# Kernel optimization log

Hardware: AMD Instinct MI355X
Metric: run time of the kernel (lower is better)

## Reference

```python
import jax, jax.numpy as jnp
import numpy as np

B, N, D = 2, 2048, 1024
H, DH = 16, 64
EPS = 1e-5


def _layernorm(t, g, b):
    m = jnp.mean(t, axis=-1, keepdims=True)
    v = jnp.mean(jnp.square(t - m), axis=-1, keepdims=True)
    return (t - m) * jax.lax.rsqrt(v + EPS) * g + b


def setup_inputs() -> dict:
    key = jax.random.key(0)
    ks = jax.random.split(key, 4)
    return {
        "x": jax.random.normal(ks[0], (B, N, D), dtype=jnp.float32),
        "ln_g": jnp.ones((D,), jnp.float32),
        "ln_b": jnp.zeros((D,), jnp.float32),
        "lnc_g": jnp.ones((D,), jnp.float32),
        "lnc_b": jnp.zeros((D,), jnp.float32),
        "Wq": jax.random.normal(ks[1], (D, H * DH), jnp.float32) * 0.02,
        "Wkv": jax.random.normal(ks[2], (D, 2 * H * DH), jnp.float32) * 0.02,
        "Wo": jax.random.normal(ks[3], (H * DH, D), jnp.float32) * 0.02,
    }


def reference(x, ln_g, ln_b, lnc_g, lnc_b, Wq, Wkv, Wo):
    scale = DH ** (-0.5)
    xn = _layernorm(x, ln_g, ln_b)          # self-attn: context = x
    cn = _layernorm(x, lnc_g, lnc_b)
    q = xn @ Wq                              # [b, n, h*d]
    kv = cn @ Wkv
    k, v = jnp.split(kv, 2, axis=-1)
    # b n (h d) -> b h n d
    q = q.reshape(B, N, H, DH).transpose(0, 2, 1, 3)
    k = k.reshape(B, N, H, DH).transpose(0, 2, 1, 3)
    v = v.reshape(B, N, H, DH).transpose(0, 2, 1, 3)
    sim = jnp.einsum("bhnd,bhmd->bhnm", q, k) * scale
    neg = -jnp.finfo(sim.dtype).max
    causal = jnp.tril(jnp.ones((N, N), dtype=bool))  # allow j <= i
    sim = jnp.where(causal[None, None], sim, neg)
    attn = jax.nn.softmax(sim.astype(jnp.float32), axis=-1)
    out = jnp.einsum("bhnm,bhmd->bhnd", attn, v)
    out = out.transpose(0, 2, 1, 3).reshape(B, N, H * DH)
    return out @ Wo
```

## Files before the change

### kernel.cpp

```cpp
#include <hip/hip_runtime.h>

#define B_  2
#define N_  2048
#define D_  1024
#define H_  16
#define DH_ 64
#define BN_ROWS (B_ * N_)
#define EPS_ 1e-5f
#define QKV_N 3072

typedef __attribute__((ext_vector_type(8))) short bf16x8_t;
typedef __attribute__((ext_vector_type(4))) float f32x4_t;

typedef const unsigned int __attribute__((address_space(1)))* gas_ptr;
typedef unsigned int __attribute__((address_space(3)))* las_ptr;

__device__ __forceinline__ void async16(const unsigned short* g, unsigned short* l) {
    __builtin_amdgcn_global_load_lds((gas_ptr)g, (las_ptr)l, 16, 0, 0);
}

__device__ __forceinline__ unsigned short f2bf(float f) {
    unsigned int u = __float_as_uint(f);
    unsigned int r = u + 0x7FFFu + ((u >> 16) & 1u);
    return (unsigned short)(r >> 16);
}

__global__ __launch_bounds__(256) void ln_dual_kernel(
    const float* __restrict__ x,
    const float* __restrict__ g1, const float* __restrict__ b1,
    const float* __restrict__ g2, const float* __restrict__ b2,
    unsigned short* __restrict__ xn, unsigned short* __restrict__ cn) {
    const int row = blockIdx.x;
    const int tid = threadIdx.x;
    const float4 v = ((const float4*)(x + (size_t)row * D_))[tid];

    float s  = v.x + v.y + v.z + v.w;
    float s2 = v.x * v.x + v.y * v.y + v.z * v.z + v.w * v.w;
    #pragma unroll
    for (int off = 32; off > 0; off >>= 1) {
        s  += __shfl_down(s,  off);
        s2 += __shfl_down(s2, off);
    }
    __shared__ float red[8];
    if ((tid & 63) == 0) { red[tid >> 6] = s; red[4 + (tid >> 6)] = s2; }
    __syncthreads();
    const float S  = red[0] + red[1] + red[2] + red[3];
    const float S2 = red[4] + red[5] + red[6] + red[7];
    const float mean = S * (1.0f / D_);
    const float var  = S2 * (1.0f / D_) - mean * mean;
    const float rstd = rsqrtf(var + EPS_);

    const float4 G1 = ((const float4*)g1)[tid];
    const float4 B1 = ((const float4*)b1)[tid];
    const float4 G2 = ((const float4*)g2)[tid];
    const float4 B2 = ((const float4*)b2)[tid];

    float nx[4] = { (v.x - mean) * rstd, (v.y - mean) * rstd,
                    (v.z - mean) * rstd, (v.w - mean) * rstd };
    ushort4 o1, o2;
    o1.x = f2bf(nx[0] * G1.x + B1.x); o1.y = f2bf(nx[1] * G1.y + B1.y);
    o1.z = f2bf(nx[2] * G1.z + B1.z); o1.w = f2bf(nx[3] * G1.w + B1.w);
    o2.x = f2bf(nx[0] * G2.x + B2.x); o2.y = f2bf(nx[1] * G2.y + B2.y);
    o2.z = f2bf(nx[2] * G2.z + B2.z); o2.w = f2bf(nx[3] * G2.w + B2.w);
    ((ushort4*)(xn + (size_t)row * D_))[tid] = o1;
    ((ushort4*)(cn + (size_t)row * D_))[tid] = o2;
}

__global__ __launch_bounds__(256) void convert_transpose_kernel(
    const float* __restrict__ in, unsigned short* __restrict__ out,
    int K, int N) {
    __shared__ float tile[32][33];
    const int n0 = blockIdx.x * 32, k0 = blockIdx.y * 32;
    const int tx = threadIdx.x, ty = threadIdx.y;
    #pragma unroll
    for (int i = 0; i < 4; i++)
        tile[ty + i * 8][tx] = in[(size_t)(k0 + ty + i * 8) * N + n0 + tx];
    __syncthreads();
    #pragma unroll
    for (int i = 0; i < 4; i++)
        out[(size_t)(n0 + ty + i * 8) * K + k0 + tx] = f2bf(tile[tx][ty + i * 8]);
}

__global__ __launch_bounds__(256) void vt_transpose_kernel(
    const unsigned short* __restrict__ qkv, unsigned short* __restrict__ vt) {
    __shared__ unsigned short tile[32][33];
    const int b = blockIdx.z;
    const int n0 = blockIdx.x * 32, c0 = blockIdx.y * 32;
    const int tx = threadIdx.x, ty = threadIdx.y;
    #pragma unroll
    for (int i = 0; i < 4; i++)
        tile[ty + i * 8][tx] =
            qkv[(size_t)(b * N_ + n0 + ty + i * 8) * QKV_N + 2048 + c0 + tx];
    __syncthreads();
    #pragma unroll
    for (int i = 0; i < 4; i++)
        vt[(size_t)(b * 1024 + c0 + ty + i * 8) * N_ + n0 + tx] = tile[tx][ty + i * 8];
}

template <bool FUSED, bool BF16OUT>
__global__ __launch_bounds__(256, 2) void gemm_kernel(
    const unsigned short* __restrict__ A0, const unsigned short* __restrict__ A1,
    const unsigned short* __restrict__ Bt, void* __restrict__ Cv,
    int M, int N, int K) {
    __shared__ unsigned short As[128 * 64];
    __shared__ unsigned short Bs[128 * 64];
    const int tid = threadIdx.x, lane = tid & 63, w = tid >> 6;
    const int quad = lane >> 4, l16 = lane & 15;
    const int lr8 = lane >> 3, pg8 = lane & 7;
    const int wr = (w >> 1) * 64, wc = (w & 1) * 64;
    const int bm = blockIdx.y * 128, bn = blockIdx.x * 128;
    const unsigned short* A = (FUSED && bn >= 1024) ? A1 : A0;

    f32x4_t acc[4][4] = {};
    for (int k0 = 0; k0 < K; k0 += 64) {
        #pragma unroll
        for (int i = 0; i < 4; i++) {
            const int rb = w * 32 + i * 8;
            const int r  = rb + lr8;
            const int g  = pg8 ^ (r & 7);
            async16(&A [(size_t)(bm + r) * K + k0 + g * 8], &As[rb * 64]);
            async16(&Bt[(size_t)(bn + r) * K + k0 + g * 8], &Bs[rb * 64]);
        }
        __syncthreads();
        #pragma unroll
        for (int kk = 0; kk < 64; kk += 32) {
            bf16x8_t af[4], bfr[4];
            const int g0 = (kk >> 3) + quad;
            #pragma unroll
            for (int t = 0; t < 4; t++)
                af[t] = *(const bf16x8_t*)&As[(wr + t * 16 + l16) * 64 +
                                              ((g0 ^ (l16 & 7)) * 8)];
            #pragma unroll
            for (int t = 0; t < 4; t++)
                bfr[t] = *(const bf16x8_t*)&Bs[(wc + t * 16 + l16) * 64 +
                                               ((g0 ^ (l16 & 7)) * 8)];
            #pragma unroll
            for (int mt = 0; mt < 4; mt++)
                #pragma unroll
                for (int nt = 0; nt < 4; nt++)
                    acc[mt][nt] = __builtin_amdgcn_mfma_f32_16x16x32_bf16(
                        af[mt], bfr[nt], acc[mt][nt], 0, 0, 0);
        }
        __syncthreads();
    }
    #pragma unroll
    for (int mt = 0; mt < 4; mt++)
        #pragma unroll
        for (int nt = 0; nt < 4; nt++)
            #pragma unroll
            for (int r = 0; r < 4; r++) {
                const int row = bm + wr + mt * 16 + quad * 4 + r;
                const int col = bn + wc + nt * 16 + l16;
                if (BF16OUT)
                    ((unsigned short*)Cv)[(size_t)row * N + col] = f2bf(acc[mt][nt][r]);
                else
                    ((float*)Cv)[(size_t)row * N + col] = acc[mt][nt][r];
            }
}

__global__ __launch_bounds__(256, 2) void flash_attn_kernel(
    const unsigned short* __restrict__ qkv, const unsigned short* __restrict__ vt,
    unsigned short* __restrict__ out) {
    __shared__ unsigned short Qs[64 * 64];
    __shared__ unsigned short Ks[64 * 64];
    __shared__ unsigned short Vts[64 * 64];
    __shared__ unsigned short Ps[4][16 * 72];

    const int tid = threadIdx.x, lane = tid & 63, w = tid >> 6;
    const int quad = lane >> 4, l16 = lane & 15;
    const int lr8 = lane >> 3, pg8 = lane & 7;
    const int pair = blockIdx.x & 15;
    const int bh = blockIdx.x >> 4;
    const int b = bh >> 4, h = bh & 15;

    const unsigned short* qb  = qkv + (size_t)(b * N_) * QKV_N + h * DH_;
    const unsigned short* kb  = qb + 1024;
    const unsigned short* vtb = vt + (size_t)(b * 1024 + h * DH_) * N_;

    constexpr float SCALE_LOG2E = 0.125f * 1.44269504088896340736f;

    for (int phase = 0; phase < 2; phase++) {
        const int qt = phase ? (31 - pair) : pair;
        const int qs = qt * 64;

        #pragma unroll
        for (int i = 0; i < 2; i++) {
            const int rb = w * 16 + i * 8;
            const int r  = rb + lr8;
            const int g  = pg8 ^ (r & 7);
            async16(&qb[(size_t)(qs + r) * QKV_N + g * 8], &Qs[rb * 64]);
        }

        f32x4_t o[4] = {};
        float ls[4] = { 0.0f, 0.0f, 0.0f, 0.0f };

        for (int jt = 0; jt <= qt; jt++) {
            const int js = jt * 64;
            #pragma unroll
            for (int i = 0; i < 2; i++) {
                const int rb = w * 16 + i * 8;
                const int r  = rb + lr8;
                const int g  = pg8 ^ (r & 7);
                async16(&kb [(size_t)(js + r) * QKV_N + g * 8], &Ks [rb * 64]);
                async16(&vtb[(size_t)r * N_ + js + g * 8],      &Vts[rb * 64]);
            }
            __syncthreads();

            f32x4_t s[4] = {};
            #pragma unroll
            for (int kk = 0; kk < 64; kk += 32) {
                const int g0 = (kk >> 3) + quad;
                const bf16x8_t a =
                    *(const bf16x8_t*)&Qs[(w * 16 + l16) * 64 + (g0 ^ (l16 & 7)) * 8];
                #pragma unroll
                for (int nt = 0; nt < 4; nt++) {
                    const bf16x8_t bb =
                        *(const bf16x8_t*)&Ks[(nt * 16 + l16) * 64 + (g0 ^ (l16 & 7)) * 8];
                    s[nt] = __builtin_amdgcn_mfma_f32_16x16x32_bf16(a, bb, s[nt], 0, 0, 0);
                }
            }

            const bool diag = (jt == qt);
            #pragma unroll
            for (int nt = 0; nt < 4; nt++)
                #pragma unroll
                for (int r = 0; r < 4; r++) {
                    float p = exp2f(s[nt][r] * SCALE_LOG2E);
                    if (diag && (js + nt * 16 + l16 > qs + w * 16 + quad * 4 + r))
                        p = 0.0f;
                    ls[r] += p;
                    Ps[w][(quad * 4 + r) * 72 + nt * 16 + l16] = f2bf(p);
                }

            #pragma unroll
            for (int kk = 0; kk < 64; kk += 32) {
                const int g0 = (kk >> 3) + quad;
                const bf16x8_t a = *(const bf16x8_t*)&Ps[w][l16 * 72 + kk + quad * 8];
                #pragma unroll
                for (int nt = 0; nt < 4; nt++) {
                    const bf16x8_t bb =
                        *(const bf16x8_t*)&Vts[(nt * 16 + l16) * 64 + (g0 ^ (l16 & 7)) * 8];
                    o[nt] = __builtin_amdgcn_mfma_f32_16x16x32_bf16(a, bb, o[nt], 0, 0, 0);
                }
            }
            __syncthreads();
        }

        #pragma unroll
        for (int off = 1; off < 16; off <<= 1)
            #pragma unroll
            for (int r = 0; r < 4; r++) ls[r] += __shfl_xor(ls[r], off);

        #pragma unroll
        for (int r = 0; r < 4; r++) {
            const float inv = 1.0f / ls[r];
            #pragma unroll
            for (int nt = 0; nt < 4; nt++) {
                const int row = b * N_ + qs + w * 16 + quad * 4 + r;
                const int col = h * DH_ + nt * 16 + l16;
                out[(size_t)row * (H_ * DH_) + col] = f2bf(o[nt][r] * inv);
            }
        }
    }
}

extern "C" void kernel_launch(void* const* d_in, const int* in_sizes, int n_in,
                              void* d_out, int out_size, void* d_ws, size_t ws_size,
                              hipStream_t stream) {
    const float* x     = (const float*)d_in[0];
    const float* ln_g  = (const float*)d_in[1];
    const float* ln_b  = (const float*)d_in[2];
    const float* lnc_g = (const float*)d_in[3];
    const float* lnc_b = (const float*)d_in[4];
    const float* Wq    = (const float*)d_in[5];
    const float* Wkv   = (const float*)d_in[6];
    const float* Wo    = (const float*)d_in[7];

    char* ws = (char*)d_ws;
    const size_t MB = 1024 * 1024;
    unsigned short* qkv   = (unsigned short*)(ws + 0 * MB);
    unsigned short* vtbuf = (unsigned short*)(ws + 24 * MB);
    unsigned short* xn    = (unsigned short*)(ws + 32 * MB);
    unsigned short* cn    = (unsigned short*)(ws + 40 * MB);
    unsigned short* wqkvT = (unsigned short*)(ws + 48 * MB);
    unsigned short* woT   = (unsigned short*)(ws + 54 * MB);
    unsigned short* ao    = xn;

    ln_dual_kernel<<<BN_ROWS, 256, 0, stream>>>(x, ln_g, ln_b, lnc_g, lnc_b, xn, cn);

    convert_transpose_kernel<<<dim3(32, 32), dim3(32, 8), 0, stream>>>(
        Wq, wqkvT, D_, 1024);
    convert_transpose_kernel<<<dim3(64, 32), dim3(32, 8), 0, stream>>>(
        Wkv, wqkvT + (size_t)1024 * 1024, D_, 2048);
    convert_transpose_kernel<<<dim3(32, 32), dim3(32, 8), 0, stream>>>(
        Wo, woT, 1024, 1024);

    gemm_kernel<true, true><<<dim3(QKV_N / 128, BN_ROWS / 128), 256, 0, stream>>>(
        xn, cn, wqkvT, qkv, BN_ROWS, QKV_N, D_);

    vt_transpose_kernel<<<dim3(64, 32, 2), dim3(32, 8), 0, stream>>>(qkv, vtbuf);

    flash_attn_kernel<<<B_ * H_ * 16, 256, 0, stream>>>(qkv, vtbuf, ao);

    gemm_kernel<false, false><<<dim3(D_ / 128, BN_ROWS / 128), 256, 0, stream>>>(
        ao, nullptr, woT, (float*)d_out, BN_ROWS, D_, H_ * DH_);
}
```

Baseline: 206.2 us.

## Enlarge attention Q tile, fold softmax scale into QKV GEMM, merge weight transposes

The flash attention kernel now processes 128 query rows per block, with 32 rows per wave. It keeps Q fragments in registers and computes S transposed so the P fragments can be written packed. The row-sum is computed with an MFMA against a ones vector instead of shuffles. The softmax scale and log2e are folded into the Q output of the QKV GEMM epilogue. The three weight-conversion launches are merged into one, and GEMM launch bounds are raised to 3 waves per SIMD. Together these aim to cut LDS traffic, ALU work and launch overhead, at the cost of fewer attention blocks (256) at occupancy 1 and a no-max softmax that relies on small scores.

```diff
diff --git a/kernel.cpp b/kernel.cpp
--- a/kernel.cpp
+++ b/kernel.cpp
@@ -1,4 +1,5 @@
 #include <hip/hip_runtime.h>
+#include <hip/hip_bf16.h>
 
 #define B_  2
 #define N_  2048
@@ -23,6 +24,11 @@
     unsigned int u = __float_as_uint(f);
     unsigned int r = u + 0x7FFFu + ((u >> 16) & 1u);
     return (unsigned short)(r >> 16);
+}
+
+__device__ __forceinline__ unsigned int pk2bf(float a, float b) {
+    __hip_bfloat162 t = __float22bfloat162_rn(float2{a, b});
+    return *(unsigned int*)&t;
 }
 
 __global__ __launch_bounds__(256) void ln_dual_kernel(
@@ -66,19 +72,29 @@
     ((ushort4*)(cn + (size_t)row * D_))[tid] = o2;
 }
 
-__global__ __launch_bounds__(256) void convert_transpose_kernel(
-    const float* __restrict__ in, unsigned short* __restrict__ out,
-    int K, int N) {
+__global__ __launch_bounds__(256) void wt_transpose_all_kernel(
+    const float* __restrict__ Wq, const float* __restrict__ Wkv,
+    const float* __restrict__ Wo,
+    unsigned short* __restrict__ wqkvT, unsigned short* __restrict__ woT) {
+    const int z = blockIdx.z;
+    const float* src;
+    unsigned short* dst;
+    int N;
+    if (z == 0)      { src = Wq;  dst = wqkvT;                        N = 1024; }
+    else if (z == 1) { src = Wkv; dst = wqkvT + (size_t)1024 * 1024;  N = 2048; }
+    else             { src = Wo;  dst = woT;                          N = 1024; }
+    const int n0 = blockIdx.x * 32, k0 = blockIdx.y * 32;
+    if (n0 >= N) return;
+
     __shared__ float tile[32][33];
-    const int n0 = blockIdx.x * 32, k0 = blockIdx.y * 32;
     const int tx = threadIdx.x, ty = threadIdx.y;
     #pragma unroll
     for (int i = 0; i < 4; i++)
-        tile[ty + i * 8][tx] = in[(size_t)(k0 + ty + i * 8) * N + n0 + tx];
+        tile[ty + i * 8][tx] = src[(size_t)(k0 + ty + i * 8) * N + n0 + tx];
     __syncthreads();
     #pragma unroll
     for (int i = 0; i < 4; i++)
-        out[(size_t)(n0 + ty + i * 8) * K + k0 + tx] = f2bf(tile[tx][ty + i * 8]);
+        dst[(size_t)(n0 + ty + i * 8) * 1024 + k0 + tx] = f2bf(tile[tx][ty + i * 8]);
 }
 
 __global__ __launch_bounds__(256) void vt_transpose_kernel(
@@ -98,7 +114,7 @@
 }
 
 template <bool FUSED, bool BF16OUT>
-__global__ __launch_bounds__(256, 2) void gemm_kernel(
+__global__ __launch_bounds__(256, 3) void gemm_kernel(
     const unsigned short* __restrict__ A0, const unsigned short* __restrict__ A1,
     const unsigned short* __restrict__ Bt, void* __restrict__ Cv,
     int M, int N, int K) {
@@ -110,6 +126,7 @@
     const int wr = (w >> 1) * 64, wc = (w & 1) * 64;
     const int bm = blockIdx.y * 128, bn = blockIdx.x * 128;
     const unsigned short* A = (FUSED && bn >= 1024) ? A1 : A0;
+    const float cscale = (FUSED && bn < 1024) ? 0.180336880111120f : 1.0f;
 
     f32x4_t acc[4][4] = {};
     for (int k0 = 0; k0 < K; k0 += 64) {
@@ -152,49 +169,54 @@
                 const int row = bm + wr + mt * 16 + quad * 4 + r;
                 const int col = bn + wc + nt * 16 + l16;
                 if (BF16OUT)
-                    ((unsigned short*)Cv)[(size_t)row * N + col] = f2bf(acc[mt][nt][r]);
+                    ((unsigned short*)Cv)[(size_t)row * N + col] =
+                        f2bf(acc[mt][nt][r] * cscale);
                 else
                     ((float*)Cv)[(size_t)row * N + col] = acc[mt][nt][r];
             }
 }
 
-__global__ __launch_bounds__(256, 2) void flash_attn_kernel(
+__global__ __launch_bounds__(256, 1) void flash_attn_kernel(
     const unsigned short* __restrict__ qkv, const unsigned short* __restrict__ vt,
     unsigned short* __restrict__ out) {
-    __shared__ unsigned short Qs[64 * 64];
+    __shared__ unsigned short Qs[128 * 64];
     __shared__ unsigned short Ks[64 * 64];
     __shared__ unsigned short Vts[64 * 64];
-    __shared__ unsigned short Ps[4][16 * 72];
+    __shared__ unsigned short Ps[4][32 * 72];
 
     const int tid = threadIdx.x, lane = tid & 63, w = tid >> 6;
     const int quad = lane >> 4, l16 = lane & 15;
     const int lr8 = lane >> 3, pg8 = lane & 7;
-    const int pair = blockIdx.x & 15;
-    const int bh = blockIdx.x >> 4;
+    const int pair = blockIdx.x & 7;
+    const int bh = blockIdx.x >> 3;
     const int b = bh >> 4, h = bh & 15;
 
     const unsigned short* qb  = qkv + (size_t)(b * N_) * QKV_N + h * DH_;
     const unsigned short* kb  = qb + 1024;
     const unsigned short* vtb = vt + (size_t)(b * 1024 + h * DH_) * N_;
 
-    constexpr float SCALE_LOG2E = 0.125f * 1.44269504088896340736f;
+    bf16x8_t ones;
+    #pragma unroll
+    for (int j = 0; j < 8; j++) ones[j] = (short)0x3F80;
 
     for (int phase = 0; phase < 2; phase++) {
-        const int qt = phase ? (31 - pair) : pair;
-        const int qs = qt * 64;
-
-        #pragma unroll
-        for (int i = 0; i < 2; i++) {
-            const int rb = w * 16 + i * 8;
+        const int qt = phase ? (15 - pair) : pair;
+        const int qs = qt * 128;
+        const int niter = 2 * qt + 2;
+
+        #pragma unroll
+        for (int i = 0; i < 4; i++) {
+            const int rb = w * 32 + i * 8;
             const int r  = rb + lr8;
             const int g  = pg8 ^ (r & 7);
             async16(&qb[(size_t)(qs + r) * QKV_N + g * 8], &Qs[rb * 64]);
         }
 
-        f32x4_t o[4] = {};
-        float ls[4] = { 0.0f, 0.0f, 0.0f, 0.0f };
-
-        for (int jt = 0; jt <= qt; jt++) {
+        f32x4_t o[2][4] = {};
+        f32x4_t lacc[2] = {};
+        bf16x8_t qf[2][2];
+
+        for (int jt = 0; jt < niter; jt++) {
             const int js = jt * 64;
             #pragma unroll
             for (int i = 0; i < 2; i++) {
@@ -206,61 +228,89 @@
             }
             __syncthreads();
 
-            f32x4_t s[4] = {};
-            #pragma unroll
-            for (int kk = 0; kk < 64; kk += 32) {
-                const int g0 = (kk >> 3) + quad;
-                const bf16x8_t a =
-                    *(const bf16x8_t*)&Qs[(w * 16 + l16) * 64 + (g0 ^ (l16 & 7)) * 8];
+            if (jt == 0) {
+                #pragma unroll
+                for (int nq = 0; nq < 2; nq++)
+                    #pragma unroll
+                    for (int k2 = 0; k2 < 2; k2++) {
+                        const int g0 = k2 * 4 + quad;
+                        qf[nq][k2] = *(const bf16x8_t*)&Qs[
+                            (w * 32 + nq * 16 + l16) * 64 + (g0 ^ (l16 & 7)) * 8];
+                    }
+            }
+
+            f32x4_t s[4][2] = {};
+            #pragma unroll
+            for (int k2 = 0; k2 < 2; k2++) {
+                const int g0 = k2 * 4 + quad;
+                #pragma unroll
+                for (int kt = 0; kt < 4; kt++) {
+                    const bf16x8_t a = *(const bf16x8_t*)&Ks[
+                        (kt * 16 + l16) * 64 + (g0 ^ (l16 & 7)) * 8];
+                    #pragma unroll
+                    for (int nq = 0; nq < 2; nq++)
+                        s[kt][nq] = __builtin_amdgcn_mfma_f32_16x16x32_bf16(
+                            a, qf[nq][k2], s[kt][nq], 0, 0, 0);
+                }
+            }
+
+            const bool edge = (jt >= niter - 2);
+            #pragma unroll
+            for (int kt = 0; kt < 4; kt++)
+                #pragma unroll
+                for (int nq = 0; nq < 2; nq++) {
+                    float p[4];
+                    #pragma unroll
+                    for (int r = 0; r < 4; r++) {
+                        float sv = s[kt][nq][r];
+                        if (edge) {
+                            const int key = js + kt * 16 + quad * 4 + r;
+                            const int qy  = qs + w * 32 + nq * 16 + l16;
+                            if (key > qy) sv = -3e38f;
+                        }
+                        p[r] = exp2f(sv);
+                    }
+                    uint2 pk = { pk2bf(p[0], p[1]), pk2bf(p[2], p[3]) };
+                    *(uint2*)&Ps[w][(nq * 16 + l16) * 72 + kt * 16 + quad * 4] = pk;
+                }
+
+            #pragma unroll
+            for (int k2 = 0; k2 < 2; k2++) {
+                const int g0 = k2 * 4 + quad;
+                bf16x8_t ap[2];
+                #pragma unroll
+                for (int mq = 0; mq < 2; mq++)
+                    ap[mq] = *(const bf16x8_t*)&Ps[w][
+                        (mq * 16 + l16) * 72 + k2 * 32 + quad * 8];
                 #pragma unroll
                 for (int nt = 0; nt < 4; nt++) {
-                    const bf16x8_t bb =
-                        *(const bf16x8_t*)&Ks[(nt * 16 + l16) * 64 + (g0 ^ (l16 & 7)) * 8];
-                    s[nt] = __builtin_amdgcn_mfma_f32_16x16x32_bf16(a, bb, s[nt], 0, 0, 0);
+                    const bf16x8_t bv = *(const bf16x8_t*)&Vts[
+                        (nt * 16 + l16) * 64 + (g0 ^ (l16 & 7)) * 8];
+                    #pragma unroll
+                    for (int mq = 0; mq < 2; mq++)
+                        o[mq][nt] = __builtin_amdgcn_mfma_f32_16x16x32_bf16(
+                            ap[mq], bv, o[mq][nt], 0, 0, 0);
                 }
-            }
-
-            const bool diag = (jt == qt);
-            #pragma unroll
-            for (int nt = 0; nt < 4; nt++)
-                #pragma unroll
-                for (int r = 0; r < 4; r++) {
-                    float p = exp2f(s[nt][r] * SCALE_LOG2E);
-                    if (diag && (js + nt * 16 + l16 > qs + w * 16 + quad * 4 + r))
-                        p = 0.0f;
-                    ls[r] += p;
-                    Ps[w][(quad * 4 + r) * 72 + nt * 16 + l16] = f2bf(p);
-                }
-
-            #pragma unroll
-            for (int kk = 0; kk < 64; kk += 32) {
-                const int g0 = (kk >> 3) + quad;
-                const bf16x8_t a = *(const bf16x8_t*)&Ps[w][l16 * 72 + kk + quad * 8];
-                #pragma unroll
-                for (int nt = 0; nt < 4; nt++) {
-                    const bf16x8_t bb =
-                        *(const bf16x8_t*)&Vts[(nt * 16 + l16) * 64 + (g0 ^ (l16 & 7)) * 8];
-                    o[nt] = __builtin_amdgcn_mfma_f32_16x16x32_bf16(a, bb, o[nt], 0, 0, 0);
-                }
+                #pragma unroll
+                for (int mq = 0; mq < 2; mq++)
+                    lacc[mq] = __builtin_amdgcn_mfma_f32_16x16x32_bf16(
+                        ap[mq], ones, lacc[mq], 0, 0, 0);
             }
             __syncthreads();
         }
 
         #pragma unroll
-        for (int off = 1; off < 16; off <<= 1)
-            #pragma unroll
-            for (int r = 0; r < 4; r++) ls[r] += __shfl_xor(ls[r], off);
-
-        #pragma unroll
-        for (int r = 0; r < 4; r++) {
-            const float inv = 1.0f / ls[r];
-            #pragma unroll
-            for (int nt = 0; nt < 4; nt++) {
-                const int row = b * N_ + qs + w * 16 + quad * 4 + r;
-                const int col = h * DH_ + nt * 16 + l16;
-                out[(size_t)row * (H_ * DH_) + col] = f2bf(o[nt][r] * inv);
-            }
-        }
+        for (int mq = 0; mq < 2; mq++)
+            #pragma unroll
+            for (int r = 0; r < 4; r++) {
+                const float inv = 1.0f / lacc[mq][r];
+                const int row = b * N_ + qs + w * 32 + mq * 16 + quad * 4 + r;
+                #pragma unroll
+                for (int nt = 0; nt < 4; nt++) {
+                    const int col = h * DH_ + nt * 16 + l16;
+                    out[(size_t)row * (H_ * DH_) + col] = f2bf(o[mq][nt][r] * inv);
+                }
+            }
     }
 }
 
@@ -288,19 +338,15 @@
 
     ln_dual_kernel<<<BN_ROWS, 256, 0, stream>>>(x, ln_g, ln_b, lnc_g, lnc_b, xn, cn);
 
-    convert_transpose_kernel<<<dim3(32, 32), dim3(32, 8), 0, stream>>>(
-        Wq, wqkvT, D_, 1024);
-    convert_transpose_kernel<<<dim3(64, 32), dim3(32, 8), 0, stream>>>(
-        Wkv, wqkvT + (size_t)1024 * 1024, D_, 2048);
-    convert_transpose_kernel<<<dim3(32, 32), dim3(32, 8), 0, stream>>>(
-        Wo, woT, 1024, 1024);
+    wt_transpose_all_kernel<<<dim3(64, 32, 3), dim3(32, 8), 0, stream>>>(
+        Wq, Wkv, Wo, wqkvT, woT);
 
     gemm_kernel<true, true><<<dim3(QKV_N / 128, BN_ROWS / 128), 256, 0, stream>>>(
         xn, cn, wqkvT, qkv, BN_ROWS, QKV_N, D_);
 
     vt_transpose_kernel<<<dim3(64, 32, 2), dim3(32, 8), 0, stream>>>(qkv, vtbuf);
 
-    flash_attn_kernel<<<B_ * H_ * 16, 256, 0, stream>>>(qkv, vtbuf, ao);
+    flash_attn_kernel<<<B_ * H_ * 8, 256, 0, stream>>>(qkv, vtbuf, ao);
 
     gemm_kernel<false, false><<<dim3(D_ / 128, BN_ROWS / 128), 256, 0, stream>>>(
         ao, nullptr, woT, (float*)d_out, BN_ROWS, D_, H_ * DH_);
```

New measurement: 222.8 us. 1.08x slower.
